# Kernel optimization log

Hardware: AMD Instinct MI355X
Metric: run time of the kernel (lower is better)

The kernel has to match this reference:

```python
import jax, jax.numpy as jnp
import numpy as np

NUM_HEADS = 8  # from init_kwargs

def _conv1x1(x, W, b):
    # x: [B, Cin, H, W], W: [Cout, Cin], b: [Cout]  (nn.Conv2d kernel_size=1)
    return jnp.einsum('bchw,oc->bohw', x, W) + b[None, :, None, None]

def setup_inputs() -> dict:
    key = jax.random.key(0)
    ks = jax.random.split(key, 9)
    B, C, H, W = 8, 256, 32, 32
    Ck, Cv, Co = 256, 256, 256
    s = 1.0 / np.sqrt(C)
    return {
        'x':  jax.random.normal(ks[0], (B, C, H, W), dtype=jnp.float32),
        'Wq': jax.random.normal(ks[1], (Ck, C), dtype=jnp.float32) * s,
        'bq': jax.random.normal(ks[2], (Ck,), dtype=jnp.float32) * 0.02,
        'Wk': jax.random.normal(ks[3], (Ck, C), dtype=jnp.float32) * s,
        'bk': jax.random.normal(ks[4], (Ck,), dtype=jnp.float32) * 0.02,
        'Wv': jax.random.normal(ks[5], (Cv, C), dtype=jnp.float32) * s,
        'bv': jax.random.normal(ks[6], (Cv,), dtype=jnp.float32) * 0.02,
        'Wo': jax.random.normal(ks[7], (Co, Cv), dtype=jnp.float32) * s,
        'bo': jax.random.normal(ks[8], (Co,), dtype=jnp.float32) * 0.02,
    }

def reference(x, Wq, bq, Wk, bk, Wv, bv, Wo, bo):
    B, C, H, W = x.shape
    q = _conv1x1(x, Wq, bq)  # [B, Ck, H, W]
    k = _conv1x1(x, Wk, bk)  # [B, Ck, H, W]
    v = _conv1x1(x, Wv, bv)  # [B, Cv, H, W]
    nh = NUM_HEADS
    dk = q.shape[1] // nh
    dv = v.shape[1] // nh
    N = H * W
    # split heads, flatten spatial dims into sequence
    q = q.reshape(B, nh, dk, N) * (dk ** -0.5)
    k = k.reshape(B, nh, dk, N)
    v = v.reshape(B, nh, dv, N)
    logits = jnp.einsum('bhdn,bhdm->bhnm', q, k)        # [B, nh, N, N]
    attn = jax.nn.softmax(logits, axis=-1)
    o = jnp.einsum('bhnm,bhdm->bhdn', attn, v)           # [B, nh, dv, N]
    o = o.reshape(B, nh * dv, H, W)
    return _conv1x1(o, Wo, bo)                           # [B, Co, H, W]
```

## Files before the change

kernel.cpp:

```cpp
#include <hip/hip_runtime.h>
#include <math.h>

typedef unsigned short u16;
typedef __attribute__((ext_vector_type(8))) unsigned short u16x8;
typedef __attribute__((ext_vector_type(8))) short s16x8;
typedef __attribute__((ext_vector_type(4))) float f32x4;

#define QK_SCALE (0.17677669529663687f * 1.4426950408889634f)

__device__ __forceinline__ unsigned cvt2(float lo, float hi) {
  unsigned r;
  asm("v_cvt_pk_bf16_f32 %0, %1, %2" : "=v"(r) : "v"(lo), "v"(hi));
  return r;
}
__device__ __forceinline__ u16 f2bf(float f) { return (u16)cvt2(f, f); }
__device__ __forceinline__ u16x8 ld16(const void* p) { u16x8 v; __builtin_memcpy(&v, p, 16); return v; }
__device__ __forceinline__ void st16(void* p, u16x8 v) { __builtin_memcpy(p, &v, 16); }
__device__ __forceinline__ void st4(void* p, unsigned v) { __builtin_memcpy(p, &v, 4); }
__device__ __forceinline__ void st8(void* p, unsigned lo, unsigned hi) {
  unsigned long long v = ((unsigned long long)hi << 32) | (unsigned long long)lo;
  __builtin_memcpy(p, &v, 8);
}
__device__ __forceinline__ f32x4 ldf4(const void* p) { f32x4 v; __builtin_memcpy(&v, p, 16); return v; }
__device__ __forceinline__ s16x8 frag16(const void* p) { s16x8 v; __builtin_memcpy(&v, p, 16); return v; }
__device__ __forceinline__ s16x8 pack8(f32x4 lo, f32x4 hi) {
  union { unsigned u[4]; s16x8 s; } c;
  c.u[0] = cvt2(lo.x, lo.y); c.u[1] = cvt2(lo.z, lo.w);
  c.u[2] = cvt2(hi.x, hi.y); c.u[3] = cvt2(hi.z, hi.w);
  return c.s;
}

__global__ __launch_bounds__(256) void r29_qkv(
    const float* __restrict__ x,
    const float* __restrict__ Wq, const float* __restrict__ bq,
    const float* __restrict__ Wk, const float* __restrict__ bk,
    const float* __restrict__ Wv, const float* __restrict__ bv,
    u16* __restrict__ qo, u16* __restrict__ ko, u16* __restrict__ vo)
{
  __shared__ u16 xt[64][264];
  __shared__ u16 wlds[192][40];

  const int t = threadIdx.x;
  const int ntile = blockIdx.x, hp = blockIdx.y, b = blockIdx.z;
  const int n0 = ntile * 64, h0 = hp * 2;
  const int w = t >> 6, lane = t & 63, l15 = lane & 15, quad = lane >> 4;
  const int oct = t & 7;

  {
    const int i = t & 15, co = t >> 4;
    const float* xb = x + ((size_t)b * 256 + co) * 1024 + n0 + i * 4;
    const int msk = (i & 7) << 3;
#pragma unroll
    for (int p = 0; p < 16; ++p) {
      const f32x4 a = ldf4(xb + (size_t)p * 16 * 1024);
      const int c = p * 16 + co;
#pragma unroll
      for (int j = 0; j < 4; ++j)
        xt[i * 4 + j][(c ^ msk)] = f2bf(a[j]);
    }
  }

  f32x4 acc[12];
#pragma unroll
  for (int i = 0; i < 12; ++i) acc[i] = (f32x4){0.f, 0.f, 0.f, 0.f};

  for (int ks = 0; ks < 8; ++ks) {
    __syncthreads();
    {
#pragma unroll
      for (int u = 0; u < 6; ++u) {
        const int row = (u * 256 + t) >> 3;
        const int m = row >> 6, hh = (row >> 5) & 1, rr = row & 31;
        const float* M = (m == 0) ? Wq : (m == 1) ? Wk : Wv;
        const f32x4 a = ldf4(M + (size_t)((h0 + hh) * 32 + rr) * 256
                             + ks * 32 + oct * 4);
        st8(&wlds[row][oct * 4], cvt2(a.x, a.y), cvt2(a.z, a.w));
      }
    }
    __syncthreads();

    const int nrow = w * 16 + l15;
    const s16x8 bfrag = frag16(
        &xt[nrow][(ks * 32 + quad * 8) ^ (((nrow >> 2) & 7) << 3)]);
#pragma unroll
    for (int mt = 0; mt < 12; ++mt) {
      const s16x8 af = frag16(&wlds[mt * 16 + l15][quad * 8]);
      acc[mt] = __builtin_amdgcn_mfma_f32_16x16x32_bf16(af, bfrag, acc[mt], 0, 0, 0);
    }
  }

  const int n = n0 + w * 16 + l15;
  const int sig = n & 127;
  const int ntn = sig >> 4, q4 = (sig >> 2) & 3, rn = sig & 3;
  const int nperm = (n & ~127) | ((ntn >> 1) << 5) | (q4 << 3) | ((ntn & 1) << 2) | rn;
#pragma unroll
  for (int hh = 0; hh < 2; ++hh) {
    const int h = h0 + hh;
    const size_t bh = (size_t)(b * 8 + h);
    u16* qrow = qo + (bh * 1024 + n) * 32;
    u16* krow = ko + (bh * 1024 + n) * 32;
#pragma unroll
    for (int half = 0; half < 2; ++half) {
      const int d0 = half * 16 + quad * 4;
      const f32x4 aq = acc[0 + hh * 2 + half];
      const f32x4 ak = acc[4 + hh * 2 + half];
      const f32x4 av = acc[8 + hh * 2 + half];
      st4(qrow + d0,     cvt2((aq.x + bq[h * 32 + d0 + 0]) * QK_SCALE,
                              (aq.y + bq[h * 32 + d0 + 1]) * QK_SCALE));
      st4(qrow + d0 + 2, cvt2((aq.z + bq[h * 32 + d0 + 2]) * QK_SCALE,
                              (aq.w + bq[h * 32 + d0 + 3]) * QK_SCALE));
      st4(krow + d0,     cvt2(ak.x + bk[h * 32 + d0 + 0],
                              ak.y + bk[h * 32 + d0 + 1]));
      st4(krow + d0 + 2, cvt2(ak.z + bk[h * 32 + d0 + 2],
                              ak.w + bk[h * 32 + d0 + 3]));
#pragma unroll
      for (int rr = 0; rr < 4; ++rr) {
        const int d = d0 + rr;
        vo[(bh * 32 + d) * 1024 + nperm] = f2bf(av[rr] + bv[h * 32 + d]);
      }
    }
  }
}

__global__ __launch_bounds__(256) void r29_attn(
    const u16* __restrict__ qw, const u16* __restrict__ kw,
    const u16* __restrict__ vw, u16* __restrict__ ows)
{
  __shared__ u16 klds[128][40];
  __shared__ u16 vlds[32][136];

  const int t = threadIdx.x;
  const int qtile = blockIdx.x;
  const int bh = blockIdx.y;
  const int w = t >> 6, lane = t & 63, l15 = lane & 15, quad = lane >> 4;

  const s16x8 qfrag = frag16(
      qw + ((size_t)bh * 1024 + qtile * 64 + w * 16 + l15) * 32 + quad * 8);

  const u16* kbase = kw + ((size_t)bh * 1024 + (t >> 1)) * 32 + (t & 1) * 16;
  const u16* vbase = vw + ((size_t)bh * 32 + (t >> 3)) * 1024 + (t & 7) * 16;

  u16x8 gk0 = ld16(kbase), gk1 = ld16(kbase + 8);
  u16x8 gv0 = ld16(vbase), gv1 = ld16(vbase + 8);

  f32x4 o0 = {0.f, 0.f, 0.f, 0.f}, o1 = {0.f, 0.f, 0.f, 0.f};
  float mrun = -1e30f, lrun = 0.f;

  for (int kb = 0; kb < 8; ++kb) {
    if (kb) __syncthreads();
    st16(&klds[t >> 1][(t & 1) * 16], gk0);
    st16(&klds[t >> 1][(t & 1) * 16 + 8], gk1);
    st16(&vlds[t >> 3][(t & 7) * 16], gv0);
    st16(&vlds[t >> 3][(t & 7) * 16 + 8], gv1);
    if (kb < 7) {
      const u16* kn = kbase + (size_t)(kb + 1) * (128 * 32);
      const u16* vn = vbase + (size_t)(kb + 1) * 128;
      gk0 = ld16(kn); gk1 = ld16(kn + 8);
      gv0 = ld16(vn); gv1 = ld16(vn + 8);
    }
    __syncthreads();

    f32x4 s[8];
    const f32x4 zz = {0.f, 0.f, 0.f, 0.f};
#pragma unroll
    for (int nt2 = 0; nt2 < 8; ++nt2) {
      const s16x8 kf = frag16(&klds[nt2 * 16 + l15][quad * 8]);
      s[nt2] = __builtin_amdgcn_mfma_f32_16x16x32_bf16(kf, qfrag, zz, 0, 0, 0);
    }

    float mx = fmaxf(fmaxf(s[0][0], s[0][1]), fmaxf(s[0][2], s[0][3]));
#pragma unroll
    for (int nt2 = 1; nt2 < 8; ++nt2)
      mx = fmaxf(mx, fmaxf(fmaxf(s[nt2][0], s[nt2][1]),
                           fmaxf(s[nt2][2], s[nt2][3])));
    mx = fmaxf(mx, __shfl_xor(mx, 16));
    mx = fmaxf(mx, __shfl_xor(mx, 32));
    const float mnew = fmaxf(mrun, mx);
    const float alpha = exp2f(mrun - mnew);
    float rs = 0.f;
#pragma unroll
    for (int nt2 = 0; nt2 < 8; ++nt2) {
#pragma unroll
      for (int r = 0; r < 4; ++r) {
        s[nt2][r] = exp2f(s[nt2][r] - mnew);
        rs += s[nt2][r];
      }
    }
    rs += __shfl_xor(rs, 16);
    rs += __shfl_xor(rs, 32);
    lrun = lrun * alpha + rs;
    mrun = mnew;
#pragma unroll
    for (int r = 0; r < 4; ++r) { o0[r] *= alpha; o1[r] *= alpha; }

#pragma unroll
    for (int ks = 0; ks < 4; ++ks) {
      const s16x8 pf  = pack8(s[2 * ks], s[2 * ks + 1]);
      const s16x8 vf0 = frag16(&vlds[l15][ks * 32 + quad * 8]);
      const s16x8 vf1 = frag16(&vlds[16 + l15][ks * 32 + quad * 8]);
      o0 = __builtin_amdgcn_mfma_f32_16x16x32_bf16(vf0, pf, o0, 0, 0, 0);
      o1 = __builtin_amdgcn_mfma_f32_16x16x32_bf16(vf1, pf, o1, 0, 0, 0);
    }
  }

  const float inv = 1.0f / lrun;
  const int b = bh >> 3, hh = bh & 7;
  u16* obase = ows + ((size_t)b * 1024 + qtile * 64 + w * 16 + l15) * 256
             + hh * 32 + quad * 4;
  st8(obase,      cvt2(o0[0] * inv, o0[1] * inv), cvt2(o0[2] * inv, o0[3] * inv));
  st8(obase + 16, cvt2(o1[0] * inv, o1[1] * inv), cvt2(o1[2] * inv, o1[3] * inv));
}

__global__ __launch_bounds__(256) void r29_oproj(
    const u16* __restrict__ ows,
    const float* __restrict__ Wo, const float* __restrict__ bo,
    float* __restrict__ out)
{
  __shared__ u16 o2t[32][256];
  __shared__ u16 wl[64][40];

  const int t = threadIdx.x;
  const int nt = blockIdx.x, b = blockIdx.y, q = blockIdx.z;
  const int w = t >> 6, lane = t & 63, l15 = lane & 15, quad = lane >> 4;

  {
    const int g = t & 31, nr = t >> 5;
#pragma unroll
    for (int p = 0; p < 4; ++p) {
      const int n = p * 8 + nr;
      const u16* src = ows + ((size_t)b * 1024 + nt * 32 + n) * 256 + g * 8;
      st16(&o2t[n][(g ^ (n & 7)) << 3], ld16(src));
    }
  }

  const int rl = t >> 2, cq = t & 3;
  const float* wsrc = Wo + (size_t)(q * 64 + rl) * 256 + cq * 8;
  unsigned wr0, wr1, wr2, wr3;
  {
    const f32x4 a = ldf4(wsrc), c = ldf4(wsrc + 4);
    wr0 = cvt2(a.x, a.y); wr1 = cvt2(a.z, a.w);
    wr2 = cvt2(c.x, c.y); wr3 = cvt2(c.z, c.w);
  }

  f32x4 acc0 = {0.f, 0.f, 0.f, 0.f}, acc1 = {0.f, 0.f, 0.f, 0.f};
  const int m0 = l15 & 7;

  for (int ks = 0; ks < 8; ++ks) {
    __syncthreads();
    st8(&wl[rl][cq * 8], wr0, wr1);
    st8(&wl[rl][cq * 8 + 4], wr2, wr3);
    __syncthreads();

    f32x4 na, nc;
    if (ks < 7) { na = ldf4(wsrc + (ks + 1) * 32); nc = ldf4(wsrc + (ks + 1) * 32 + 4); }

    const s16x8 af = frag16(&wl[w * 16 + l15][quad * 8]);
    const s16x8 b0 = frag16(&o2t[l15][((ks * 4 + quad) ^ m0) << 3]);
    const s16x8 b1 = frag16(&o2t[16 + l15][((ks * 4 + quad) ^ m0) << 3]);
    acc0 = __builtin_amdgcn_mfma_f32_16x16x32_bf16(af, b0, acc0, 0, 0, 0);
    acc1 = __builtin_amdgcn_mfma_f32_16x16x32_bf16(af, b1, acc1, 0, 0, 0);

    if (ks < 7) {
      wr0 = cvt2(na.x, na.y); wr1 = cvt2(na.z, na.w);
      wr2 = cvt2(nc.x, nc.y); wr3 = cvt2(nc.z, nc.w);
    }
  }

#pragma unroll
  for (int r = 0; r < 4; ++r) {
    const int oc = q * 64 + w * 16 + quad * 4 + r;
    const float bov = bo[oc];
    out[((size_t)b * 256 + oc) * 1024 + nt * 32 + l15]      = acc0[r] + bov;
    out[((size_t)b * 256 + oc) * 1024 + nt * 32 + 16 + l15] = acc1[r] + bov;
  }
}

extern "C" void kernel_launch(void* const* d_in, const int* in_sizes, int n_in,
                              void* d_out, int out_size, void* d_ws, size_t ws_size,
                              hipStream_t stream) {
  (void)in_sizes; (void)n_in; (void)out_size; (void)ws_size;
  const float* x  = (const float*)d_in[0];
  const float* Wq = (const float*)d_in[1];
  const float* bq = (const float*)d_in[2];
  const float* Wk = (const float*)d_in[3];
  const float* bk = (const float*)d_in[4];
  const float* Wv = (const float*)d_in[5];
  const float* bv = (const float*)d_in[6];
  const float* Wo = (const float*)d_in[7];
  const float* bo = (const float*)d_in[8];
  float* out = (float*)d_out;

  char* ws = (char*)d_ws;
  u16* qw  = (u16*)(ws);
  u16* kw  = (u16*)(ws + (4u << 20));
  u16* vw  = (u16*)(ws + (8u << 20));
  u16* ows = (u16*)(ws + (12u << 20));

  r29_qkv<<<dim3(16, 4, 8), 256, 0, stream>>>(
      x, Wq, bq, Wk, bk, Wv, bv, qw, kw, vw);
  r29_attn<<<dim3(16, 64), 256, 0, stream>>>(qw, kw, vw, ows);
  r29_oproj<<<dim3(32, 8, 4), 256, 0, stream>>>(ows, Wo, bo, out);
}
```

Measured before the change: 127.4 us.

## Double-buffer attention LDS tiles, remap block order, and raise MFMA priority

The attention kernel now keeps two LDS buffers for K and V. This removes the barrier at the start of each key block, so the next tile can be stored while other waves still compute on the current one. The grid is flattened to 1D and remapped so that consecutive blocks cover 8 heads of the same query tile, which is meant to improve cache locality for K and V. s_setprio is raised around the MFMA sections to favour matrix issue across waves. The cost is doubled LDS use, which may lower occupancy.

```diff
diff --git a/kernel.cpp b/kernel.cpp
--- a/kernel.cpp
+++ b/kernel.cpp
@@ -30,7 +30,7 @@
   return c.s;
 }
 
-__global__ __launch_bounds__(256) void r29_qkv(
+__global__ __launch_bounds__(256) void r30_qkv(
     const float* __restrict__ x,
     const float* __restrict__ Wq, const float* __restrict__ bq,
     const float* __restrict__ Wk, const float* __restrict__ bk,
@@ -122,16 +122,17 @@
   }
 }
 
-__global__ __launch_bounds__(256) void r29_attn(
+__global__ __launch_bounds__(256) void r30_attn(
     const u16* __restrict__ qw, const u16* __restrict__ kw,
     const u16* __restrict__ vw, u16* __restrict__ ows)
 {
-  __shared__ u16 klds[128][40];
-  __shared__ u16 vlds[32][136];
+  __shared__ u16 klds[2][128][40];
+  __shared__ u16 vlds[2][32][136];
 
   const int t = threadIdx.x;
-  const int qtile = blockIdx.x;
-  const int bh = blockIdx.y;
+  const int id = blockIdx.x;
+  const int qtile = (id >> 3) & 15;
+  const int bh = (id & 7) + ((id >> 7) << 3);
   const int w = t >> 6, lane = t & 63, l15 = lane & 15, quad = lane >> 4;
 
   const s16x8 qfrag = frag16(
@@ -147,11 +148,11 @@
   float mrun = -1e30f, lrun = 0.f;
 
   for (int kb = 0; kb < 8; ++kb) {
-    if (kb) __syncthreads();
-    st16(&klds[t >> 1][(t & 1) * 16], gk0);
-    st16(&klds[t >> 1][(t & 1) * 16 + 8], gk1);
-    st16(&vlds[t >> 3][(t & 7) * 16], gv0);
-    st16(&vlds[t >> 3][(t & 7) * 16 + 8], gv1);
+    const int cur = kb & 1;
+    st16(&klds[cur][t >> 1][(t & 1) * 16], gk0);
+    st16(&klds[cur][t >> 1][(t & 1) * 16 + 8], gk1);
+    st16(&vlds[cur][t >> 3][(t & 7) * 16], gv0);
+    st16(&vlds[cur][t >> 3][(t & 7) * 16 + 8], gv1);
     if (kb < 7) {
       const u16* kn = kbase + (size_t)(kb + 1) * (128 * 32);
       const u16* vn = vbase + (size_t)(kb + 1) * 128;
@@ -162,11 +163,13 @@
 
     f32x4 s[8];
     const f32x4 zz = {0.f, 0.f, 0.f, 0.f};
+    __builtin_amdgcn_s_setprio(1);
 #pragma unroll
     for (int nt2 = 0; nt2 < 8; ++nt2) {
-      const s16x8 kf = frag16(&klds[nt2 * 16 + l15][quad * 8]);
+      const s16x8 kf = frag16(&klds[cur][nt2 * 16 + l15][quad * 8]);
       s[nt2] = __builtin_amdgcn_mfma_f32_16x16x32_bf16(kf, qfrag, zz, 0, 0, 0);
     }
+    __builtin_amdgcn_s_setprio(0);
 
     float mx = fmaxf(fmaxf(s[0][0], s[0][1]), fmaxf(s[0][2], s[0][3]));
 #pragma unroll
@@ -193,14 +196,16 @@
 #pragma unroll
     for (int r = 0; r < 4; ++r) { o0[r] *= alpha; o1[r] *= alpha; }
 
+    __builtin_amdgcn_s_setprio(1);
 #pragma unroll
     for (int ks = 0; ks < 4; ++ks) {
       const s16x8 pf  = pack8(s[2 * ks], s[2 * ks + 1]);
-      const s16x8 vf0 = frag16(&vlds[l15][ks * 32 + quad * 8]);
-      const s16x8 vf1 = frag16(&vlds[16 + l15][ks * 32 + quad * 8]);
+      const s16x8 vf0 = frag16(&vlds[cur][l15][ks * 32 + quad * 8]);
+      const s16x8 vf1 = frag16(&vlds[cur][16 + l15][ks * 32 + quad * 8]);
       o0 = __builtin_amdgcn_mfma_f32_16x16x32_bf16(vf0, pf, o0, 0, 0, 0);
       o1 = __builtin_amdgcn_mfma_f32_16x16x32_bf16(vf1, pf, o1, 0, 0, 0);
     }
+    __builtin_amdgcn_s_setprio(0);
   }
 
   const float inv = 1.0f / lrun;
@@ -211,7 +216,7 @@
   st8(obase + 16, cvt2(o1[0] * inv, o1[1] * inv), cvt2(o1[2] * inv, o1[3] * inv));
 }
 
-__global__ __launch_bounds__(256) void r29_oproj(
+__global__ __launch_bounds__(256) void r30_oproj(
     const u16* __restrict__ ows,
     const float* __restrict__ Wo, const float* __restrict__ bo,
     float* __restrict__ out)
@@ -296,8 +301,8 @@
   u16* vw  = (u16*)(ws + (8u << 20));
   u16* ows = (u16*)(ws + (12u << 20));
 
-  r29_qkv<<<dim3(16, 4, 8), 256, 0, stream>>>(
+  r30_qkv<<<dim3(16, 4, 8), 256, 0, stream>>>(
       x, Wq, bq, Wk, bk, Wv, bv, qw, kw, vw);
-  r29_attn<<<dim3(16, 64), 256, 0, stream>>>(qw, kw, vw, ows);
-  r29_oproj<<<dim3(32, 8, 4), 256, 0, stream>>>(ows, Wo, bo, out);
-}
+  r30_attn<<<dim3(1024), 256, 0, stream>>>(qw, kw, vw, ows);
+  r30_oproj<<<dim3(32, 8, 4), 256, 0, stream>>>(ows, Wo, bo, out);
+}
```

New measurement: 125.4 us. No clear change (-1.6%).

## Split attention KV range across two blocks and merge partials

Applied to the files above, without the earlier changes.

The attention kernel now processes half the key/value sequence per block, doubling the grid to 2048 blocks with a remapped block index. Each block writes unnormalized fp32 partial outputs plus running max and sum, and a new merge kernel rescales and combines them into the bf16 output. It also adds MFMA priority hints and moves the prefetch after the barrier. This gains occupancy and parallelism, paid for by an extra launch and fp32 partial traffic of about 16MB written and read back.

```diff
diff --git a/kernel.cpp b/kernel.cpp
--- a/kernel.cpp
+++ b/kernel.cpp
@@ -22,6 +22,7 @@
   __builtin_memcpy(p, &v, 8);
 }
 __device__ __forceinline__ f32x4 ldf4(const void* p) { f32x4 v; __builtin_memcpy(&v, p, 16); return v; }
+__device__ __forceinline__ void stf4(void* p, f32x4 v) { __builtin_memcpy(p, &v, 16); }
 __device__ __forceinline__ s16x8 frag16(const void* p) { s16x8 v; __builtin_memcpy(&v, p, 16); return v; }
 __device__ __forceinline__ s16x8 pack8(f32x4 lo, f32x4 hi) {
   union { unsigned u[4]; s16x8 s; } c;
@@ -30,7 +31,7 @@
   return c.s;
 }
 
-__global__ __launch_bounds__(256) void r29_qkv(
+__global__ __launch_bounds__(256) void r33_qkv(
     const float* __restrict__ x,
     const float* __restrict__ Wq, const float* __restrict__ bq,
     const float* __restrict__ Wk, const float* __restrict__ bk,
@@ -122,23 +123,26 @@
   }
 }
 
-__global__ __launch_bounds__(256) void r29_attn(
+__global__ __launch_bounds__(256) void r33_attn_split(
     const u16* __restrict__ qw, const u16* __restrict__ kw,
-    const u16* __restrict__ vw, u16* __restrict__ ows)
+    const u16* __restrict__ vw, float* __restrict__ pf,
+    float* __restrict__ ml)
 {
   __shared__ u16 klds[128][40];
   __shared__ u16 vlds[32][136];
 
   const int t = threadIdx.x;
-  const int qtile = blockIdx.x;
-  const int bh = blockIdx.y;
+  const int id = blockIdx.x;
+  const int qtile = (id >> 3) & 15;
+  const int half = (id >> 7) & 1;
+  const int bh = (id & 7) + ((id >> 8) << 3);
   const int w = t >> 6, lane = t & 63, l15 = lane & 15, quad = lane >> 4;
 
   const s16x8 qfrag = frag16(
       qw + ((size_t)bh * 1024 + qtile * 64 + w * 16 + l15) * 32 + quad * 8);
 
-  const u16* kbase = kw + ((size_t)bh * 1024 + (t >> 1)) * 32 + (t & 1) * 16;
-  const u16* vbase = vw + ((size_t)bh * 32 + (t >> 3)) * 1024 + (t & 7) * 16;
+  const u16* kbase = kw + ((size_t)bh * 1024 + half * 512 + (t >> 1)) * 32 + (t & 1) * 16;
+  const u16* vbase = vw + ((size_t)bh * 32 + (t >> 3)) * 1024 + half * 512 + (t & 7) * 16;
 
   u16x8 gk0 = ld16(kbase), gk1 = ld16(kbase + 8);
   u16x8 gv0 = ld16(vbase), gv1 = ld16(vbase + 8);
@@ -146,27 +150,30 @@
   f32x4 o0 = {0.f, 0.f, 0.f, 0.f}, o1 = {0.f, 0.f, 0.f, 0.f};
   float mrun = -1e30f, lrun = 0.f;
 
-  for (int kb = 0; kb < 8; ++kb) {
+  for (int kb = 0; kb < 4; ++kb) {
     if (kb) __syncthreads();
     st16(&klds[t >> 1][(t & 1) * 16], gk0);
     st16(&klds[t >> 1][(t & 1) * 16 + 8], gk1);
     st16(&vlds[t >> 3][(t & 7) * 16], gv0);
     st16(&vlds[t >> 3][(t & 7) * 16 + 8], gv1);
-    if (kb < 7) {
+    __syncthreads();
+
+    if (kb < 3) {
       const u16* kn = kbase + (size_t)(kb + 1) * (128 * 32);
       const u16* vn = vbase + (size_t)(kb + 1) * 128;
       gk0 = ld16(kn); gk1 = ld16(kn + 8);
       gv0 = ld16(vn); gv1 = ld16(vn + 8);
     }
-    __syncthreads();
 
     f32x4 s[8];
     const f32x4 zz = {0.f, 0.f, 0.f, 0.f};
+    __builtin_amdgcn_s_setprio(1);
 #pragma unroll
     for (int nt2 = 0; nt2 < 8; ++nt2) {
       const s16x8 kf = frag16(&klds[nt2 * 16 + l15][quad * 8]);
       s[nt2] = __builtin_amdgcn_mfma_f32_16x16x32_bf16(kf, qfrag, zz, 0, 0, 0);
     }
+    __builtin_amdgcn_s_setprio(0);
 
     float mx = fmaxf(fmaxf(s[0][0], s[0][1]), fmaxf(s[0][2], s[0][3]));
 #pragma unroll
@@ -193,25 +200,59 @@
 #pragma unroll
     for (int r = 0; r < 4; ++r) { o0[r] *= alpha; o1[r] *= alpha; }
 
+    __builtin_amdgcn_s_setprio(1);
 #pragma unroll
     for (int ks = 0; ks < 4; ++ks) {
-      const s16x8 pf  = pack8(s[2 * ks], s[2 * ks + 1]);
+      const s16x8 pfr = pack8(s[2 * ks], s[2 * ks + 1]);
       const s16x8 vf0 = frag16(&vlds[l15][ks * 32 + quad * 8]);
       const s16x8 vf1 = frag16(&vlds[16 + l15][ks * 32 + quad * 8]);
-      o0 = __builtin_amdgcn_mfma_f32_16x16x32_bf16(vf0, pf, o0, 0, 0, 0);
-      o1 = __builtin_amdgcn_mfma_f32_16x16x32_bf16(vf1, pf, o1, 0, 0, 0);
-    }
-  }
-
-  const float inv = 1.0f / lrun;
+      o0 = __builtin_amdgcn_mfma_f32_16x16x32_bf16(vf0, pfr, o0, 0, 0, 0);
+      o1 = __builtin_amdgcn_mfma_f32_16x16x32_bf16(vf1, pfr, o1, 0, 0, 0);
+    }
+    __builtin_amdgcn_s_setprio(0);
+  }
+
   const int b = bh >> 3, hh = bh & 7;
-  u16* obase = ows + ((size_t)b * 1024 + qtile * 64 + w * 16 + l15) * 256
-             + hh * 32 + quad * 4;
-  st8(obase,      cvt2(o0[0] * inv, o0[1] * inv), cvt2(o0[2] * inv, o0[3] * inv));
-  st8(obase + 16, cvt2(o1[0] * inv, o1[1] * inv), cvt2(o1[2] * inv, o1[3] * inv));
-}
-
-__global__ __launch_bounds__(256) void r29_oproj(
+  const int n = qtile * 64 + w * 16 + l15;
+  float* pbase = pf + (((size_t)half * 8 + b) * 1024 + n) * 256 + hh * 32 + quad * 4;
+  stf4(pbase, o0);
+  stf4(pbase + 16, o1);
+  if (quad == 0) {
+    float* mlp = ml + ((size_t)half * 65536 + (size_t)bh * 1024 + n) * 2;
+    mlp[0] = mrun;
+    mlp[1] = lrun;
+  }
+}
+
+__global__ __launch_bounds__(256) void r33_merge(
+    const float* __restrict__ pf, const float* __restrict__ ml,
+    u16* __restrict__ ows)
+{
+  const int t = threadIdx.x, g = blockIdx.x;
+#pragma unroll
+  for (int u = 0; u < 2; ++u) {
+    const int idx = g * 512 + u * 256 + t;
+    const int c4 = idx & 63;
+    const int bn = idx >> 6;
+    const int b = bn >> 10, n = bn & 1023;
+    const int hh = c4 >> 3;
+    const size_t mlo = ((size_t)b * 8 + hh) * 1024 + n;
+    const float m1 = ml[mlo * 2], l1 = ml[mlo * 2 + 1];
+    const float m2 = ml[(65536 + mlo) * 2], l2 = ml[(65536 + mlo) * 2 + 1];
+    const float M = fmaxf(m1, m2);
+    const float s1 = exp2f(m1 - M), s2 = exp2f(m2 - M);
+    const float inv = 1.0f / (s1 * l1 + s2 * l2);
+    const size_t po = (size_t)bn * 256 + c4 * 4;
+    const f32x4 p1 = ldf4(pf + po);
+    const f32x4 p2 = ldf4(pf + 2097152 + po);
+    f32x4 o;
+#pragma unroll
+    for (int r = 0; r < 4; ++r) o[r] = (s1 * p1[r] + s2 * p2[r]) * inv;
+    st8(ows + po, cvt2(o.x, o.y), cvt2(o.z, o.w));
+  }
+}
+
+__global__ __launch_bounds__(256) void r33_oproj(
     const u16* __restrict__ ows,
     const float* __restrict__ Wo, const float* __restrict__ bo,
     float* __restrict__ out)
@@ -291,13 +332,16 @@
   float* out = (float*)d_out;
 
   char* ws = (char*)d_ws;
-  u16* qw  = (u16*)(ws);
-  u16* kw  = (u16*)(ws + (4u << 20));
-  u16* vw  = (u16*)(ws + (8u << 20));
-  u16* ows = (u16*)(ws + (12u << 20));
-
-  r29_qkv<<<dim3(16, 4, 8), 256, 0, stream>>>(
+  u16*   qw  = (u16*)(ws);
+  u16*   kw  = (u16*)(ws + (4u << 20));
+  u16*   vw  = (u16*)(ws + (8u << 20));
+  u16*   ows = (u16*)(ws + (12u << 20));
+  float* pf  = (float*)(ws + (16u << 20));
+  float* ml  = (float*)(ws + (32u << 20));
+
+  r33_qkv<<<dim3(16, 4, 8), 256, 0, stream>>>(
       x, Wq, bq, Wk, bk, Wv, bv, qw, kw, vw);
-  r29_attn<<<dim3(16, 64), 256, 0, stream>>>(qw, kw, vw, ows);
-  r29_oproj<<<dim3(32, 8, 4), 256, 0, stream>>>(ows, Wo, bo, out);
-}
+  r33_attn_split<<<dim3(2048), 256, 0, stream>>>(qw, kw, vw, pf, ml);
+  r33_merge<<<dim3(1024), 256, 0, stream>>>(pf, ml, ows);
+  r33_oproj<<<dim3(32, 8, 4), 256, 0, stream>>>(ows, Wo, bo, out);
+}
```

Result: slower. 133.6 us (+4.9%).
